# Optimization experiments

Hardware: AMD Instinct MI355X
Metric: run time of the kernel (lower is better)

## Reference

```python
import jax, jax.numpy as jnp
import numpy as np

B, S, E, G = 64, 24, 128, 256
Km, Kch, Ko, Kp, Kc = 100, 200, 50, 50, 30
Vm, Vch, Vo, Vp, Vl, Vc = 1000, 3000, 500, 1500, 700, 2000
Veth, Vgen, Vage, Vins = 10, 2, 100, 5
TOTK = Km + Kch + Ko + Kp + 1 + Kc + 4  # 435 concat width


def setup_inputs() -> dict:
    key = jax.random.key(0)
    ks = jax.random.split(key, 24)
    ri = lambda k, shape, hi: jax.random.randint(k, shape, 0, hi)
    rn = lambda k, shape: (jax.random.normal(k, shape, dtype=jnp.float32) * 0.02)
    return {
        'meds': ri(ks[0], (B, S, Km), Vm),
        'chart': ri(ks[1], (B, S, Kch), Vch),
        'out': ri(ks[2], (B, S, Ko), Vo),
        'proc': ri(ks[3], (B, S, Kp), Vp),
        'lab': ri(ks[4], (B, S), Vl),
        'conds': ri(ks[5], (B, Kc), Vc),
        'demo': ri(ks[6], (B, 4), 2),
        'med_E': rn(ks[7], (Vm, E)), 'chart_E': rn(ks[8], (Vch, E)),
        'out_E': rn(ks[9], (Vo, E)), 'proc_E': rn(ks[10], (Vp, E)),
        'lab_E': rn(ks[11], (Vl, E)), 'cond_E': rn(ks[12], (Vc, E)),
        'gender_E': rn(ks[13], (Vgen, E)), 'eth_E': rn(ks[14], (Veth, E)),
        'ins_E': rn(ks[15], (Vins, E)), 'age_E': rn(ks[16], (Vage, E)),
        'proj_W': rn(ks[17], (TOTK, E)), 'proj_b': jnp.zeros((E,), jnp.float32),
        'W1': rn(ks[18], (E, G)), 'b1': jnp.zeros((G,), jnp.float32),
        'W2': rn(ks[19], (G, G)), 'b2': jnp.zeros((G,), jnp.float32),
        'fc1_W': rn(ks[20], (G, G // 2)), 'fc1_b': jnp.zeros((G // 2,), jnp.float32),
        'fc2_W': rn(ks[21], (G // 2, 1)), 'fc2_b': jnp.zeros((1,), jnp.float32),
    }


def _forward(meds, chart, out, proc, lab, conds, demo,
             med_E, chart_E, out_E, proc_E, lab_E, cond_E,
             gender_E, eth_E, ins_E, age_E,
             proj_W, proj_b, W1, b1, W2, b2, fc1_W, fc1_b, fc2_W, fc2_b):
    clamp = lambda i, V: jnp.clip(i, 0, V - 1)
    med_e = med_E[clamp(meds, Vm)]        # [B,S,Km,E]
    chart_e = chart_E[clamp(chart, Vch)]  # [B,S,Kch,E]
    out_e = out_E[clamp(out, Vo)]         # [B,S,Ko,E]
    proc_e = proc_E[clamp(proc, Vp)]      # [B,S,Kp,E]
    lab_e = lab_E[clamp(lab, Vl)]         # [B,S,E]
    cond_e = cond_E[clamp(conds, Vc)]     # [B,Kc,E]
    gen_e = gender_E[demo[:, 0]]          # [B,E]
    eth_e = eth_E[demo[:, 1]]
    ins_e = ins_E[demo[:, 2]]
    age_e = age_E[demo[:, 3]]
    demo_cols = [jnp.broadcast_to(d[:, None, :, None], (B, S, E, 1))
                 for d in (gen_e, eth_e, ins_e, age_e)]
    x = jnp.concatenate([
        med_e.transpose(0, 1, 3, 2),    # [B,S,E,Km]
        chart_e.transpose(0, 1, 3, 2),
        out_e.transpose(0, 1, 3, 2),
        proc_e.transpose(0, 1, 3, 2),
        lab_e[..., None],               # [B,S,E,1]
        jnp.broadcast_to(cond_e[:, None], (B, S, Kc, E)).transpose(0, 1, 3, 2),
    ] + demo_cols, axis=-1)             # [B,S,E,TOTK]
    x = x.mean(axis=-2)                 # mean over embed dim -> [B,S,TOTK]
    N = B * S
    x = x.reshape(N, TOTK) @ proj_W + proj_b   # [N,E]
    # GCNConv over complete graph + self loops: normalized adjacency is 1/N
    # everywhere, so aggregation == node-mean of (x @ W).
    h = jnp.broadcast_to(jnp.mean(x @ W1, axis=0, keepdims=True) + b1, (N, G))
    h = jax.nn.relu(h)
    # entropy attention
    w = jnp.exp(-jnp.sum(h * jnp.log(h + 1e-9), axis=1))
    h = h * (w / jnp.sum(w))[:, None]
    h = jnp.broadcast_to(jnp.mean(h @ W2, axis=0, keepdims=True) + b2, (N, G))
    x_pooled = h.reshape(B, S, G).mean(axis=1)          # [B,G]
    f = jax.nn.relu(x_pooled @ fc1_W + fc1_b)           # [B,G/2]
    o = f @ fc2_W + fc2_b                               # [B,1]
    return jax.nn.sigmoid(o), o


def reference(meds, chart, out, proc, lab, conds, demo,
              med_E, chart_E, out_E, proc_E, lab_E, cond_E,
              gender_E, eth_E, ins_E, age_E,
              proj_W, proj_b, W1, b1, W2, b2, fc1_W, fc1_b, fc2_W, fc2_b):
    return _forward(meds, chart, out, proc, lab, conds, demo,
                    med_E, chart_E, out_E, proc_E, lab_E, cond_E,
                    gender_E, eth_E, ins_E, age_E,
                    proj_W, proj_b, W1, b1, W2, b2, fc1_W, fc1_b, fc2_W, fc2_b)
```

## Files before the change

### kernel.cpp

```cpp
#include <hip/hip_runtime.h>
#include <math.h>

#define B_ 64
#define S_ 24
#define E_ 128
#define G_ 256
#define N_ (B_ * S_)
#define Km_ 100
#define Kch_ 200
#define Ko_ 50
#define Kp_ 50
#define Kc_ 30
#define TOTK_ 435

#define Vm_ 1000
#define Vch_ 3000
#define Vo_ 500
#define Vp_ 1500
#define Vl_ 700
#define Vc_ 2000
#define Vgen_ 2
#define Veth_ 10
#define Vins_ 5
#define Vage_ 100
#define TOTROWS_ 8817

#define OFF_MED 0
#define OFF_CHART 1000
#define OFF_OUT 4000
#define OFF_PROC 4500
#define OFF_LAB 6000
#define OFF_COND 6700
#define OFF_GEN 8700
#define OFF_ETH 8702
#define OFF_INS 8712
#define OFF_AGE 8717
#define OFF_MACC 8817

__global__ __launch_bounds__(256) void rowmeans_kernel(
    const float* __restrict__ medE, const float* __restrict__ chartE,
    const float* __restrict__ outE, const float* __restrict__ procE,
    const float* __restrict__ labE, const float* __restrict__ condE,
    const float* __restrict__ genE, const float* __restrict__ ethE,
    const float* __restrict__ insE, const float* __restrict__ ageE,
    float* __restrict__ rm)
{
    int wave = (blockIdx.x * blockDim.x + threadIdx.x) >> 6;
    int lane = threadIdx.x & 63;
    if (wave >= TOTROWS_) return;

    const float* src;
    int r = wave;
    if (r < Vm_)                  { src = medE; }
    else if ((r -= Vm_)  < Vch_)  { src = chartE; }
    else if ((r -= Vch_) < Vo_)   { src = outE; }
    else if ((r -= Vo_)  < Vp_)   { src = procE; }
    else if ((r -= Vp_)  < Vl_)   { src = labE; }
    else if ((r -= Vl_)  < Vc_)   { src = condE; }
    else if ((r -= Vc_)  < Vgen_) { src = genE; }
    else if ((r -= Vgen_)< Veth_) { src = ethE; }
    else if ((r -= Veth_)< Vins_) { src = insE; }
    else                          { r -= Vins_; src = ageE; }

    float2 v = *reinterpret_cast<const float2*>(src + (size_t)r * E_ + lane * 2);
    float s = v.x + v.y;
    #pragma unroll
    for (int off = 32; off > 0; off >>= 1) s += __shfl_down(s, off, 64);
    if (lane == 0) rm[wave] = s * (1.0f / E_);
}

__device__ __forceinline__ int clampi(int v, int hi) {
    return v < 0 ? 0 : (v > hi ? hi : v);
}

__global__ __launch_bounds__(256) void colsum_kernel(
    const int* __restrict__ meds, const int* __restrict__ chart,
    const int* __restrict__ outv, const int* __restrict__ proc,
    const int* __restrict__ lab,  const int* __restrict__ conds,
    const int* __restrict__ demo,
    const float* __restrict__ rm, float* __restrict__ macc)
{
    const int c = blockIdx.x;
    const int t = threadIdx.x;
    float s = 0.0f;
    float scale;

    if (c < 400) {
        const int* idx; int K, kk, base, vmax;
        if (c < Km_)             { idx = meds;  K = Km_;  kk = c;        base = OFF_MED;  vmax = Vm_ - 1; }
        else if (c < 300)        { idx = chart; K = Kch_; kk = c - 100;  base = OFF_CHART;vmax = Vch_ - 1; }
        else if (c < 350)        { idx = outv;  K = Ko_;  kk = c - 300;  base = OFF_OUT;  vmax = Vo_ - 1; }
        else                     { idx = proc;  K = Kp_;  kk = c - 350;  base = OFF_PROC; vmax = Vp_ - 1; }
        for (int n = t; n < N_; n += 256)
            s += rm[base + clampi(idx[n * K + kk], vmax)];
        scale = 1.0f / N_;
    } else if (c == 400) {
        for (int n = t; n < N_; n += 256)
            s += rm[OFF_LAB + clampi(lab[n], Vl_ - 1)];
        scale = 1.0f / N_;
    } else if (c < 431) {
        int kk = c - 401;
        for (int b = t; b < B_; b += 256)
            s += rm[OFF_COND + clampi(conds[b * Kc_ + kk], Vc_ - 1)];
        scale = 1.0f / B_;
    } else {
        int j = c - 431;
        int base = (j == 0) ? OFF_GEN : (j == 1) ? OFF_ETH : (j == 2) ? OFF_INS : OFF_AGE;
        for (int b = t; b < B_; b += 256)
            s += rm[base + demo[b * 4 + j]];
        scale = 1.0f / B_;
    }

    __shared__ float red[256];
    red[t] = s;
    __syncthreads();
    #pragma unroll
    for (int off = 128; off > 0; off >>= 1) {
        if (t < off) red[t] += red[t + off];
        __syncthreads();
    }
    if (t == 0) macc[c] = red[0] * scale;
}

__global__ __launch_bounds__(512) void head_kernel(
    const float* __restrict__ macc,
    const float* __restrict__ projW, const float* __restrict__ projb,
    const float* __restrict__ W1, const float* __restrict__ b1,
    const float* __restrict__ W2, const float* __restrict__ b2,
    const float* __restrict__ fc1W, const float* __restrict__ fc1b,
    const float* __restrict__ fc2W, const float* __restrict__ fc2b,
    float* __restrict__ outp)
{
    __shared__ float sm[TOTK_];
    __shared__ float xbar[E_];
    __shared__ float h1s[G_];
    __shared__ float h2s[G_];
    __shared__ float fsh[G_ / 2];
    __shared__ float4 part4[8][64];
    __shared__ float2 part2[8][64];
    __shared__ float red[8];
    __shared__ float oval;

    const int t = threadIdx.x;
    const int lane = t & 63;
    const int oc = t >> 6;

    for (int i = t; i < TOTK_; i += 512) sm[i] = macc[i];
    __syncthreads();

    {
        const float2* Wp = (const float2*)projW;
        const int k0 = (TOTK_ * oc) >> 3;
        const int k1 = (TOTK_ * (oc + 1)) >> 3;
        float2 acc = {0.f, 0.f};
        #pragma unroll 8
        for (int k = k0; k < k1; ++k) {
            float s = sm[k];
            float2 w = Wp[k * 64 + lane];
            acc.x += s * w.x; acc.y += s * w.y;
        }
        part2[oc][lane] = acc;
        __syncthreads();
        if (t < 64) {
            float2 a = part2[0][t];
            #pragma unroll
            for (int j = 1; j < 8; ++j) { a.x += part2[j][t].x; a.y += part2[j][t].y; }
            xbar[2 * t]     = a.x + projb[2 * t];
            xbar[2 * t + 1] = a.y + projb[2 * t + 1];
        }
        __syncthreads();
    }

    {
        const float4* Wp = (const float4*)W1;
        const int k0 = oc * 16, k1 = k0 + 16;
        float4 acc = {0.f, 0.f, 0.f, 0.f};
        #pragma unroll 8
        for (int k = k0; k < k1; ++k) {
            float s = xbar[k];
            float4 w = Wp[k * 64 + lane];
            acc.x += s * w.x; acc.y += s * w.y; acc.z += s * w.z; acc.w += s * w.w;
        }
        part4[oc][lane] = acc;
        __syncthreads();
        if (t < 64) {
            float4 a = part4[0][t];
            #pragma unroll
            for (int j = 1; j < 8; ++j) {
                float4 p = part4[j][t];
                a.x += p.x; a.y += p.y; a.z += p.z; a.w += p.w;
            }
            float4 bb = ((const float4*)b1)[t];
            h1s[4 * t]     = fmaxf(a.x + bb.x, 0.f) * (1.0f / N_);
            h1s[4 * t + 1] = fmaxf(a.y + bb.y, 0.f) * (1.0f / N_);
            h1s[4 * t + 2] = fmaxf(a.z + bb.z, 0.f) * (1.0f / N_);
            h1s[4 * t + 3] = fmaxf(a.w + bb.w, 0.f) * (1.0f / N_);
        }
        __syncthreads();
    }

    {
        const float4* Wp = (const float4*)W2;
        const int k0 = oc * 32, k1 = k0 + 32;
        float4 acc = {0.f, 0.f, 0.f, 0.f};
        #pragma unroll 8
        for (int k = k0; k < k1; ++k) {
            float s = h1s[k];
            float4 w = Wp[k * 64 + lane];
            acc.x += s * w.x; acc.y += s * w.y; acc.z += s * w.z; acc.w += s * w.w;
        }
        part4[oc][lane] = acc;
        __syncthreads();
        if (t < 64) {
            float4 a = part4[0][t];
            #pragma unroll
            for (int j = 1; j < 8; ++j) {
                float4 p = part4[j][t];
                a.x += p.x; a.y += p.y; a.z += p.z; a.w += p.w;
            }
            float4 bb = ((const float4*)b2)[t];
            h2s[4 * t]     = a.x + bb.x;
            h2s[4 * t + 1] = a.y + bb.y;
            h2s[4 * t + 2] = a.z + bb.z;
            h2s[4 * t + 3] = a.w + bb.w;
        }
        __syncthreads();
    }

    {
        const float2* Wp = (const float2*)fc1W;
        const int k0 = oc * 32, k1 = k0 + 32;
        float2 acc = {0.f, 0.f};
        #pragma unroll 8
        for (int k = k0; k < k1; ++k) {
            float s = h2s[k];
            float2 w = Wp[k * 64 + lane];
            acc.x += s * w.x; acc.y += s * w.y;
        }
        part2[oc][lane] = acc;
        __syncthreads();
        if (t < 64) {
            float2 a = part2[0][t];
            #pragma unroll
            for (int j = 1; j < 8; ++j) { a.x += part2[j][t].x; a.y += part2[j][t].y; }
            fsh[2 * t]     = fmaxf(a.x + fc1b[2 * t], 0.f);
            fsh[2 * t + 1] = fmaxf(a.y + fc1b[2 * t + 1], 0.f);
        }
        __syncthreads();
    }

    {
        float p = (t < G_ / 2) ? fsh[t] * fc2W[t] : 0.f;
        #pragma unroll
        for (int off = 32; off > 0; off >>= 1) p += __shfl_down(p, off, 64);
        if (lane == 0) red[oc] = p;
        __syncthreads();
        if (t == 0) {
            float o = fc2b[0];
            #pragma unroll
            for (int j = 0; j < 8; ++j) o += red[j];
            oval = o;
        }
        __syncthreads();
        const float o = oval;
        const float sig = 1.0f / (1.0f + expf(-o));
        if (t < B_)            outp[t] = sig;
        else if (t < 2 * B_)   outp[t] = o;
    }
}

extern "C" void kernel_launch(void* const* d_in, const int* in_sizes, int n_in,
                              void* d_out, int out_size, void* d_ws, size_t ws_size,
                              hipStream_t stream) {
    const int* meds  = (const int*)d_in[0];
    const int* chart = (const int*)d_in[1];
    const int* outv  = (const int*)d_in[2];
    const int* proc  = (const int*)d_in[3];
    const int* lab   = (const int*)d_in[4];
    const int* conds = (const int*)d_in[5];
    const int* demo  = (const int*)d_in[6];
    const float* medE   = (const float*)d_in[7];
    const float* chartE = (const float*)d_in[8];
    const float* outE   = (const float*)d_in[9];
    const float* procE  = (const float*)d_in[10];
    const float* labE   = (const float*)d_in[11];
    const float* condE  = (const float*)d_in[12];
    const float* genE   = (const float*)d_in[13];
    const float* ethE   = (const float*)d_in[14];
    const float* insE   = (const float*)d_in[15];
    const float* ageE   = (const float*)d_in[16];
    const float* projW  = (const float*)d_in[17];
    const float* projb  = (const float*)d_in[18];
    const float* W1     = (const float*)d_in[19];
    const float* b1     = (const float*)d_in[20];
    const float* W2     = (const float*)d_in[21];
    const float* b2     = (const float*)d_in[22];
    const float* fc1W   = (const float*)d_in[23];
    const float* fc1b   = (const float*)d_in[24];
    const float* fc2W   = (const float*)d_in[25];
    const float* fc2b   = (const float*)d_in[26];

    float* rm   = (float*)d_ws;
    float* macc = rm + OFF_MACC;
    float* outp = (float*)d_out;

    int blocksA = (TOTROWS_ + 3) / 4;
    rowmeans_kernel<<<blocksA, 256, 0, stream>>>(
        medE, chartE, outE, procE, labE, condE, genE, ethE, insE, ageE, rm);

    colsum_kernel<<<TOTK_, 256, 0, stream>>>(
        meds, chart, outv, proc, lab, conds, demo, rm, macc);

    head_kernel<<<1, 512, 0, stream>>>(
        macc, projW, projb, W1, b1, W2, b2, fc1W, fc1b, fc2W, fc2b, outp);
}
```

Before: 31.05 us.

## Fuse column-sum and head into one kernel using a last-block atomic counter

Merges the column-sum and head kernels into a single 65-block launch. The last block to finish, detected with an atomic counter and thread fences, runs the MLP head. The column-sum work is reorganized into 16 row-chunks per table, with threads mapped across index columns so idx reads are coalesced, and partial sums go to a workspace that the head reduces. This removes one kernel launch and the strided per-column gathers. In exchange it adds an atomic, fences, and a serialized tail block, and the row-mean kernel now uses 512-thread blocks and resets the counter.

```diff
diff --git a/kernel.cpp b/kernel.cpp
--- a/kernel.cpp
+++ b/kernel.cpp
@@ -19,10 +19,6 @@
 #define Vp_ 1500
 #define Vl_ 700
 #define Vc_ 2000
-#define Vgen_ 2
-#define Veth_ 10
-#define Vins_ 5
-#define Vage_ 100
 #define TOTROWS_ 8817
 
 #define OFF_MED 0
@@ -35,95 +31,80 @@
 #define OFF_ETH 8702
 #define OFF_INS 8712
 #define OFF_AGE 8717
-#define OFF_MACC 8817
-
-__global__ __launch_bounds__(256) void rowmeans_kernel(
+#define OFF_CTR 8824
+#define OFF_PART 8832
+
+#define NCHUNK_ 16
+#define CHUNK_N_ 96
+#define NBLK_B_ 65
+#define NTHR_ 512
+
+__device__ __forceinline__ int clampi(int v, int hi) {
+    return v < 0 ? 0 : (v > hi ? hi : v);
+}
+
+__global__ __launch_bounds__(NTHR_) void rowmeans_kernel(
     const float* __restrict__ medE, const float* __restrict__ chartE,
     const float* __restrict__ outE, const float* __restrict__ procE,
     const float* __restrict__ labE, const float* __restrict__ condE,
     const float* __restrict__ genE, const float* __restrict__ ethE,
     const float* __restrict__ insE, const float* __restrict__ ageE,
-    float* __restrict__ rm)
+    float* __restrict__ rm, int* __restrict__ ctr)
 {
-    int wave = (blockIdx.x * blockDim.x + threadIdx.x) >> 6;
+    if (blockIdx.x == 0 && threadIdx.x == 0) *ctr = 0;
+
+    int row = blockIdx.x * (NTHR_ / 64) + (threadIdx.x >> 6);
     int lane = threadIdx.x & 63;
-    if (wave >= TOTROWS_) return;
+    if (row >= TOTROWS_) return;
 
     const float* src;
-    int r = wave;
+    int r = row;
     if (r < Vm_)                  { src = medE; }
     else if ((r -= Vm_)  < Vch_)  { src = chartE; }
     else if ((r -= Vch_) < Vo_)   { src = outE; }
     else if ((r -= Vo_)  < Vp_)   { src = procE; }
     else if ((r -= Vp_)  < Vl_)   { src = labE; }
     else if ((r -= Vl_)  < Vc_)   { src = condE; }
-    else if ((r -= Vc_)  < Vgen_) { src = genE; }
-    else if ((r -= Vgen_)< Veth_) { src = ethE; }
-    else if ((r -= Veth_)< Vins_) { src = insE; }
-    else                          { r -= Vins_; src = ageE; }
+    else if ((r -= Vc_)  < 2)     { src = genE; }
+    else if ((r -= 2)    < 10)    { src = ethE; }
+    else if ((r -= 10)   < 5)     { src = insE; }
+    else                          { r -= 5; src = ageE; }
 
     float2 v = *reinterpret_cast<const float2*>(src + (size_t)r * E_ + lane * 2);
     float s = v.x + v.y;
     #pragma unroll
     for (int off = 32; off > 0; off >>= 1) s += __shfl_down(s, off, 64);
-    if (lane == 0) rm[wave] = s * (1.0f / E_);
-}
-
-__device__ __forceinline__ int clampi(int v, int hi) {
-    return v < 0 ? 0 : (v > hi ? hi : v);
-}
-
-__global__ __launch_bounds__(256) void colsum_kernel(
-    const int* __restrict__ meds, const int* __restrict__ chart,
-    const int* __restrict__ outv, const int* __restrict__ proc,
-    const int* __restrict__ lab,  const int* __restrict__ conds,
-    const int* __restrict__ demo,
-    const float* __restrict__ rm, float* __restrict__ macc)
+    if (lane == 0) rm[row] = s * (1.0f / E_);
+}
+
+template<int K, int RPI, int CBASE, int RMBASE, int VMAX>
+__device__ __forceinline__ void table_chunk(
+    const int* __restrict__ idx, const float* __restrict__ rm,
+    float* __restrict__ part, int p, int t, float* __restrict__ lds)
 {
-    const int c = blockIdx.x;
-    const int t = threadIdx.x;
-    float s = 0.0f;
-    float scale;
-
-    if (c < 400) {
-        const int* idx; int K, kk, base, vmax;
-        if (c < Km_)             { idx = meds;  K = Km_;  kk = c;        base = OFF_MED;  vmax = Vm_ - 1; }
-        else if (c < 300)        { idx = chart; K = Kch_; kk = c - 100;  base = OFF_CHART;vmax = Vch_ - 1; }
-        else if (c < 350)        { idx = outv;  K = Ko_;  kk = c - 300;  base = OFF_OUT;  vmax = Vo_ - 1; }
-        else                     { idx = proc;  K = Kp_;  kk = c - 350;  base = OFF_PROC; vmax = Vp_ - 1; }
-        for (int n = t; n < N_; n += 256)
-            s += rm[base + clampi(idx[n * K + kk], vmax)];
-        scale = 1.0f / N_;
-    } else if (c == 400) {
-        for (int n = t; n < N_; n += 256)
-            s += rm[OFF_LAB + clampi(lab[n], Vl_ - 1)];
-        scale = 1.0f / N_;
-    } else if (c < 431) {
-        int kk = c - 401;
-        for (int b = t; b < B_; b += 256)
-            s += rm[OFF_COND + clampi(conds[b * Kc_ + kk], Vc_ - 1)];
-        scale = 1.0f / B_;
-    } else {
-        int j = c - 431;
-        int base = (j == 0) ? OFF_GEN : (j == 1) ? OFF_ETH : (j == 2) ? OFF_INS : OFF_AGE;
-        for (int b = t; b < B_; b += 256)
-            s += rm[base + demo[b * 4 + j]];
-        scale = 1.0f / B_;
-    }
-
-    __shared__ float red[256];
-    red[t] = s;
+    constexpr int ACT = K * RPI;
+    float acc = 0.0f;
+    if (t < ACT) {
+        const int kk = t % K;
+        const int nr = t / K;
+        const int n0 = p * CHUNK_N_;
+        for (int n = n0 + nr; n < n0 + CHUNK_N_; n += RPI) {
+            int ix = clampi(idx[n * K + kk], VMAX);
+            acc += rm[RMBASE + ix];
+        }
+    }
+    lds[t] = acc;
     __syncthreads();
-    #pragma unroll
-    for (int off = 128; off > 0; off >>= 1) {
-        if (t < off) red[t] += red[t + off];
-        __syncthreads();
-    }
-    if (t == 0) macc[c] = red[0] * scale;
-}
-
-__global__ __launch_bounds__(512) void head_kernel(
-    const float* __restrict__ macc,
+    if (t < K) {
+        float s = lds[t];
+        #pragma unroll
+        for (int r = 1; r < RPI; ++r) s += lds[r * K + t];
+        part[(CBASE + t) * NCHUNK_ + p] = s;
+    }
+}
+
+__device__ void head_body(
+    const float* __restrict__ part,
     const float* __restrict__ projW, const float* __restrict__ projb,
     const float* __restrict__ W1, const float* __restrict__ b1,
     const float* __restrict__ W2, const float* __restrict__ b2,
@@ -138,14 +119,28 @@
     __shared__ float fsh[G_ / 2];
     __shared__ float4 part4[8][64];
     __shared__ float2 part2[8][64];
-    __shared__ float red[8];
+    __shared__ float hred[8];
     __shared__ float oval;
 
     const int t = threadIdx.x;
     const int lane = t & 63;
     const int oc = t >> 6;
 
-    for (int i = t; i < TOTK_; i += 512) sm[i] = macc[i];
+    if (t < TOTK_) {
+        const float4* pp = (const float4*)(part + t * NCHUNK_);
+        float s;
+        if (t < 400) {
+            float4 a = pp[0], b = pp[1], c = pp[2], d = pp[3];
+            s = (((a.x + a.y) + (a.z + a.w)) + ((b.x + b.y) + (b.z + b.w)))
+              + (((c.x + c.y) + (c.z + c.w)) + ((d.x + d.y) + (d.z + d.w)));
+            s *= (1.0f / N_);
+        } else if (t == 400) {
+            s = part[t * NCHUNK_] * (1.0f / N_);
+        } else {
+            s = part[t * NCHUNK_] * (1.0f / B_);
+        }
+        sm[t] = s;
+    }
     __syncthreads();
 
     {
@@ -253,12 +248,12 @@
         float p = (t < G_ / 2) ? fsh[t] * fc2W[t] : 0.f;
         #pragma unroll
         for (int off = 32; off > 0; off >>= 1) p += __shfl_down(p, off, 64);
-        if (lane == 0) red[oc] = p;
+        if (lane == 0) hred[oc] = p;
         __syncthreads();
         if (t == 0) {
             float o = fc2b[0];
             #pragma unroll
-            for (int j = 0; j < 8; ++j) o += red[j];
+            for (int j = 0; j < 8; ++j) o += hred[j];
             oval = o;
         }
         __syncthreads();
@@ -266,6 +261,67 @@
         const float sig = 1.0f / (1.0f + expf(-o));
         if (t < B_)            outp[t] = sig;
         else if (t < 2 * B_)   outp[t] = o;
+    }
+}
+
+__global__ __launch_bounds__(NTHR_) void colsum_head_kernel(
+    const int* __restrict__ meds, const int* __restrict__ chart,
+    const int* __restrict__ outv, const int* __restrict__ proc,
+    const int* __restrict__ lab,  const int* __restrict__ conds,
+    const int* __restrict__ demo,
+    const float* __restrict__ rm, float* __restrict__ part, int* __restrict__ ctr,
+    const float* __restrict__ projW, const float* __restrict__ projb,
+    const float* __restrict__ W1, const float* __restrict__ b1,
+    const float* __restrict__ W2, const float* __restrict__ b2,
+    const float* __restrict__ fc1W, const float* __restrict__ fc1b,
+    const float* __restrict__ fc2W, const float* __restrict__ fc2b,
+    float* __restrict__ outp)
+{
+    __shared__ float lds_red[NTHR_];
+    __shared__ int s_old;
+
+    const int t = threadIdx.x;
+    const int bid = blockIdx.x;
+
+    if (bid < 64) {
+        const int table = bid >> 4;
+        const int p = bid & 15;
+        if (table == 0)      table_chunk<Km_, 5, 0,   OFF_MED,  Vm_ -1>(meds,  rm, part, p, t, lds_red);
+        else if (table == 1) table_chunk<Kch_,2, 100, OFF_CHART,Vch_-1>(chart, rm, part, p, t, lds_red);
+        else if (table == 2) table_chunk<Ko_, 10,300, OFF_OUT,  Vo_ -1>(outv,  rm, part, p, t, lds_red);
+        else                 table_chunk<Kp_, 10,350, OFF_PROC, Vp_ -1>(proc,  rm, part, p, t, lds_red);
+    } else {
+        const int lane = t & 63;
+        const int w = t >> 6;
+        for (int j = w; j < 35; j += 8) {
+            float s = 0.0f;
+            if (j == 0) {
+                #pragma unroll
+                for (int i = 0; i < 24; ++i)
+                    s += rm[OFF_LAB + clampi(lab[lane + 64 * i], Vl_ - 1)];
+            } else if (j < 31) {
+                int kk = j - 1;
+                s = rm[OFF_COND + clampi(conds[lane * Kc_ + kk], Vc_ - 1)];
+            } else {
+                int jj = j - 31;
+                int base = (jj == 0) ? OFF_GEN : (jj == 1) ? OFF_ETH :
+                           (jj == 2) ? OFF_INS : OFF_AGE;
+                s = rm[base + demo[lane * 4 + jj]];
+            }
+            #pragma unroll
+            for (int off = 32; off > 0; off >>= 1) s += __shfl_down(s, off, 64);
+            if (lane == 0) part[(400 + j) * NCHUNK_] = s;
+        }
+    }
+
+    __threadfence();
+    __syncthreads();
+    if (t == 0) s_old = atomicAdd(ctr, 1);
+    __syncthreads();
+    if (s_old == NBLK_B_ - 1) {
+        __threadfence();
+        head_body(part, projW, projb, W1, b1, W2, b2,
+                  fc1W, fc1b, fc2W, fc2b, outp);
     }
 }
 
@@ -301,16 +357,15 @@
     const float* fc2b   = (const float*)d_in[26];
 
     float* rm   = (float*)d_ws;
-    float* macc = rm + OFF_MACC;
+    int*   ctr  = (int*)d_ws + OFF_CTR;
+    float* part = (float*)d_ws + OFF_PART;
     float* outp = (float*)d_out;
 
-    int blocksA = (TOTROWS_ + 3) / 4;
-    rowmeans_kernel<<<blocksA, 256, 0, stream>>>(
-        medE, chartE, outE, procE, labE, condE, genE, ethE, insE, ageE, rm);
-
-    colsum_kernel<<<TOTK_, 256, 0, stream>>>(
-        meds, chart, outv, proc, lab, conds, demo, rm, macc);
-
-    head_kernel<<<1, 512, 0, stream>>>(
-        macc, projW, projb, W1, b1, W2, b2, fc1W, fc1b, fc2W, fc2b, outp);
-}
+    int blocksA = (TOTROWS_ + (NTHR_ / 64) - 1) / (NTHR_ / 64);
+    rowmeans_kernel<<<blocksA, NTHR_, 0, stream>>>(
+        medE, chartE, outE, procE, labE, condE, genE, ethE, insE, ageE, rm, ctr);
+
+    colsum_head_kernel<<<NBLK_B_, NTHR_, 0, stream>>>(
+        meds, chart, outv, proc, lab, conds, demo, rm, part, ctr,
+        projW, projb, W1, b1, W2, b2, fc1W, fc1b, fc2W, fc2b, outp);
+}
```

After: 38.62 us. 1.24x slower.
